# Kernel tuning notes

Measured on AMD Instinct MI355X. Metric: run time of the kernel, lower is better.

## Reference

```python
import jax, jax.numpy as jnp
import numpy as np

# Module/problem constants (match init_kwargs & input_specs)
B, D, H, W = 2, 96, 96, 96
CIN, COUT, K = 16, 32, 3
N = 200000  # number of active (sparse) voxels


def setup_inputs() -> dict:
    key = jax.random.key(0)
    kf, kw, kb = jax.random.split(key, 3)
    # unique valid voxel coordinates -> deterministic scatter semantics
    rng = np.random.default_rng(0)
    lin = rng.choice(B * D * H * W, size=N, replace=False)
    b, z, y, x = np.unravel_index(lin, (B, D, H, W))
    indices = jnp.asarray(np.stack([b, z, y, x], axis=1).astype(np.int32))  # [N,4]
    features = jax.random.normal(kf, (N, CIN), dtype=jnp.float32)
    fan_in = CIN * K ** 3
    conv_w = jax.random.normal(kw, (COUT, CIN, K, K, K), dtype=jnp.float32) / np.sqrt(fan_in)
    conv_b = jax.random.normal(kb, (COUT,), dtype=jnp.float32) * 0.01
    return {"features": features, "indices": indices, "conv_w": conv_w, "conv_b": conv_b}


def reference(features, indices, conv_w, conv_b):
    """DenseFallbackConv3d.forward on a SparseConvTensor, stride=1 path.

    1) scatter sparse features into dense grid [B,CIN,D,H,W]
    2) dense Conv3d (k=3, pad=1, stride=1) + bias
    3) gather per-point output features at the same voxel indices -> [N,COUT]
    """
    b = indices[:, 0]
    z = indices[:, 1]
    y = indices[:, 2]
    x = indices[:, 3]
    # scatter: equivalent of grid[b, :, z, y, x] = features
    grid = jnp.zeros((B, CIN, D, H, W), dtype=features.dtype).at[b, :, z, y, x].set(features)
    out = jax.lax.conv_general_dilated(
        grid, conv_w,
        window_strides=(1, 1, 1),
        padding=((1, 1), (1, 1), (1, 1)),
        dimension_numbers=("NCDHW", "OIDHW", "NCDHW"),
    )
    out = out + conv_b[None, :, None, None, None]
    # gather: out_dense[b, :, z, y, x] for every active voxel -> [N, COUT]
    return out[b, :, z, y, x]
```

## Files before the change

### kernel.cpp

```cpp
#include <hip/hip_runtime.h>

#define BB   2
#define DD   96
#define HH   96
#define WW   96
#define CINC 16
#define COUTC 32
#define KVOL 27
#define GRID_VOX (BB*DD*HH*WW)
#define NW (KVOL*CINC*COUTC)
#define VPT 8
#define CVB (256*VPT)

typedef _Float16 half8 __attribute__((ext_vector_type(8)));
typedef float    floatx16 __attribute__((ext_vector_type(16)));

__global__ __launch_bounds__(256) void setup_kernel(
        const int* __restrict__ idx, int* __restrict__ g,
        const float* __restrict__ w, _Float16* __restrict__ wH,
        int* __restrict__ counter, int n, int scatter_blocks) {
    if ((int)blockIdx.x < scatter_blocks) {
        int i = blockIdx.x * 256 + threadIdx.x;
        if (i >= n) return;
        int4 v = ((const int4*)idx)[i];
        int lin = ((v.x * DD + v.y) * HH + v.z) * WW + v.w;
        g[lin] = i;
    } else {
        int t = ((int)blockIdx.x - scatter_blocks) * 256 + threadIdx.x;
        if (t == 0) counter[0] = 0;
        if (t >= NW) return;
        int ci = t & (CINC - 1);
        int co = (t >> 4) & (COUTC - 1);
        int kk = t >> 9;
        wH[t] = (_Float16)w[(co * CINC + ci) * KVOL + kk];
    }
}

__global__ __launch_bounds__(256) void compact_kernel(
        const int* __restrict__ idx, const float* __restrict__ feat,
        int* __restrict__ g, _Float16* __restrict__ featH,
        int* __restrict__ pc, int* __restrict__ perm,
        int* __restrict__ counter, int n) {
    __shared__ int s_off[256];
    __shared__ int s_base;
    const int t = threadIdx.x;
    const int base = blockIdx.x * CVB + t * VPT;

    int4 a0 = ((const int4*)(g + base))[0];
    int4 a1 = ((const int4*)(g + base))[1];
    int vals[VPT] = {a0.x, a0.y, a0.z, a0.w, a1.x, a1.y, a1.z, a1.w};
    int pid[VPT], pck[VPT];
    int cnt = 0;
#pragma unroll
    for (int q = 0; q < VPT; ++q) {
        int p = vals[q];
        bool ok = ((unsigned)p < (unsigned)n);
        int pk = 0;
        if (ok) {
            int4 c = ((const int4*)idx)[p];
            int lin = ((c.x * DD + c.y) * HH + c.z) * WW + c.w;
            ok = (lin == base + q);
            pk = (c.x << 21) | (c.y << 14) | (c.z << 7) | c.w;
        }
        pid[q] = ok ? p : -1;
        pck[q] = pk;
        cnt += ok ? 1 : 0;
    }

    s_off[t] = cnt;
    __syncthreads();
    for (int d = 1; d < 256; d <<= 1) {
        int v = (t >= d) ? s_off[t - d] : 0;
        __syncthreads();
        s_off[t] += v;
        __syncthreads();
    }
    if (t == 255) s_base = atomicAdd(counter, s_off[255]);
    __syncthreads();
    int o = s_base + s_off[t] - cnt;

#pragma unroll
    for (int q = 0; q < VPT; ++q) {
        int tag = n;
        int p = pid[q];
        if (p >= 0) {
            pc[o] = pck[q];
            perm[o] = p;
            const float4* src = (const float4*)(feat + (size_t)p * CINC);
            float4 f0 = src[0], f1 = src[1], f2 = src[2], f3 = src[3];
            half8 h0, h1;
            h0[0]=(_Float16)f0.x; h0[1]=(_Float16)f0.y; h0[2]=(_Float16)f0.z; h0[3]=(_Float16)f0.w;
            h0[4]=(_Float16)f1.x; h0[5]=(_Float16)f1.y; h0[6]=(_Float16)f1.z; h0[7]=(_Float16)f1.w;
            h1[0]=(_Float16)f2.x; h1[1]=(_Float16)f2.y; h1[2]=(_Float16)f2.z; h1[3]=(_Float16)f2.w;
            h1[4]=(_Float16)f3.x; h1[5]=(_Float16)f3.y; h1[6]=(_Float16)f3.z; h1[7]=(_Float16)f3.w;
            half8* dst = (half8*)(featH + (size_t)o * CINC);
            dst[0] = h0; dst[1] = h1;
            tag = o;
            ++o;
        }
        g[base + q] = tag;
    }
    if (blockIdx.x == 0 && t == 0) {
        half8* zr = (half8*)(featH + (size_t)n * CINC);
        half8 hz = {};
        zr[0] = hz; zr[1] = hz;
    }
}

__global__ __launch_bounds__(256) void conv_mfma_kernel(
        const _Float16* __restrict__ featH, const int* __restrict__ pc,
        const int* __restrict__ perm, const _Float16* __restrict__ wH,
        const float* __restrict__ bias, const int* __restrict__ g,
        float* __restrict__ out, int n) {
    const int lane = threadIdx.x & 63;
    const int wave = threadIdx.x >> 6;
    const int m    = lane & 31;
    const int hf   = lane >> 5;
    const int j0   = (blockIdx.x * 4 + wave) * 32;
    if (j0 >= n) return;
    const int j = j0 + m;

    const int p = pc[j];
    const int x = p & 127, y = (p >> 7) & 127, z = (p >> 14) & 127, b = p >> 21;
    const int base = ((b * DD + z) * HH + y) * WW + x;
    const int pm = perm[j];

    int nid[KVOL];
#pragma unroll
    for (int kk = 0; kk < KVOL; ++kk) {
        const int dz = kk / 9 - 1, dy = (kk / 3) % 3 - 1, dx = kk % 3 - 1;
        int nz = z + dz, ny = y + dy, nx = x + dx;
        bool inb = ((unsigned)nz < DD) & ((unsigned)ny < HH) & ((unsigned)nx < WW);
        int addr = inb ? base + (dz * HH + dy) * WW + dx : 0;
        int v = g[addr];
        nid[kk] = inb ? v : n;
    }

    float bval = bias[m];
    floatx16 acc;
#pragma unroll
    for (int i = 0; i < 16; ++i) acc[i] = bval;

#pragma unroll
    for (int kk = 0; kk < KVOL; ++kk) {
        half8 a = *(const half8*)(featH + (size_t)nid[kk] * CINC + hf * 8);
        half8 bf = *(const half8*)(wH + kk * (COUTC * CINC) + m * CINC + hf * 8);
        acc = __builtin_amdgcn_mfma_f32_32x32x16_f16(a, bf, acc, 0, 0, 0);
    }

#pragma unroll
    for (int i = 0; i < 16; ++i) {
        int r = (i & 3) + 8 * (i >> 2) + 4 * hf;
        int row = __shfl(pm, r);
        out[(size_t)row * COUTC + m] = acc[i];
    }
}

extern "C" void kernel_launch(void* const* d_in, const int* in_sizes, int n_in,
                              void* d_out, int out_size, void* d_ws, size_t ws_size,
                              hipStream_t stream) {
    const float* feat  = (const float*)d_in[0];
    const int*   idx   = (const int*)d_in[1];
    const float* convw = (const float*)d_in[2];
    const float* convb = (const float*)d_in[3];
    float* out = (float*)d_out;

    const int n = in_sizes[1] / 4;

    char* ws = (char*)d_ws;
    int*      g       = (int*)ws;
    int*      counter = (int*)(ws + GRID_VOX * 4);
    int*      pc      = (int*)(ws + GRID_VOX * 4 + 256);
    int*      perm    = pc + n;
    _Float16* featH   = (_Float16*)(perm + n);
    _Float16* wH      = featH + (size_t)(n + 1) * CINC;

    hipMemsetAsync(g, 0xFF, (size_t)GRID_VOX * sizeof(int), stream);

    const int sb = (n + 255) / 256;
    const int rb = (NW + 255) / 256;
    setup_kernel<<<sb + rb, 256, 0, stream>>>(idx, g, convw, wH, counter, n, sb);
    compact_kernel<<<GRID_VOX / CVB, 256, 0, stream>>>(
        idx, feat, g, featH, pc, perm, counter, n);

    const int waves = (n + 31) / 32;
    conv_mfma_kernel<<<(waves + 3) / 4, 256, 0, stream>>>(
        featH, pc, perm, wH, convb, g, out, n);
}
```

Measured before the change: 127.9 us.

## Stage weights in LDS, batch neighbor loads, use wave scan, and drop grid memset

The conv kernel now copies the fp16 weights into padded shared memory once per block and reads the B operand from LDS. It also issues the nine neighbor feature loads of each group before their MFMAs, so more loads are in flight at once. The compaction kernel replaces its LDS Hillis-Steele scan, which had many barriers, with a wave-level shuffle scan plus a 4-entry combine. The memset of the dense index grid is removed, relying on the existing idx-based validation to reject stale or garbage entries. The trade-off is an LDS-fill prologue per block and higher register pressure from holding nine feature vectors.

```diff
diff --git a/kernel.cpp b/kernel.cpp
--- a/kernel.cpp
+++ b/kernel.cpp
@@ -11,6 +11,7 @@
 #define NW (KVOL*CINC*COUTC)
 #define VPT 8
 #define CVB (256*VPT)
+#define SWP 24
 
 typedef _Float16 half8 __attribute__((ext_vector_type(8)));
 typedef float    floatx16 __attribute__((ext_vector_type(16)));
@@ -41,9 +42,12 @@
         int* __restrict__ g, _Float16* __restrict__ featH,
         int* __restrict__ pc, int* __restrict__ perm,
         int* __restrict__ counter, int n) {
-    __shared__ int s_off[256];
+    __shared__ int s_wsum[4];
+    __shared__ int s_wbase[4];
     __shared__ int s_base;
     const int t = threadIdx.x;
+    const int lane = t & 63;
+    const int wv = t >> 6;
     const int base = blockIdx.x * CVB + t * VPT;
 
     int4 a0 = ((const int4*)(g + base))[0];
@@ -67,17 +71,22 @@
         cnt += ok ? 1 : 0;
     }
 
-    s_off[t] = cnt;
+    int incl = cnt;
+#pragma unroll
+    for (int d = 1; d < 64; d <<= 1) {
+        int v = __shfl_up(incl, d);
+        if (lane >= d) incl += v;
+    }
+    if (lane == 63) s_wsum[wv] = incl;
     __syncthreads();
-    for (int d = 1; d < 256; d <<= 1) {
-        int v = (t >= d) ? s_off[t - d] : 0;
-        __syncthreads();
-        s_off[t] += v;
-        __syncthreads();
-    }
-    if (t == 255) s_base = atomicAdd(counter, s_off[255]);
+    if (t == 0) {
+        int t0 = s_wsum[0], t1 = s_wsum[1], t2 = s_wsum[2], t3 = s_wsum[3];
+        s_wbase[0] = 0; s_wbase[1] = t0; s_wbase[2] = t0 + t1;
+        s_wbase[3] = t0 + t1 + t2;
+        s_base = atomicAdd(counter, t0 + t1 + t2 + t3);
+    }
     __syncthreads();
-    int o = s_base + s_off[t] - cnt;
+    int o = s_base + s_wbase[wv] + incl - cnt;
 
 #pragma unroll
     for (int q = 0; q < VPT; ++q) {
@@ -112,11 +121,21 @@
         const int* __restrict__ perm, const _Float16* __restrict__ wH,
         const float* __restrict__ bias, const int* __restrict__ g,
         float* __restrict__ out, int n) {
+    __shared__ _Float16 sW[KVOL * 32 * SWP];
     const int lane = threadIdx.x & 63;
     const int wave = threadIdx.x >> 6;
     const int m    = lane & 31;
     const int hf   = lane >> 5;
-    const int j0   = (blockIdx.x * 4 + wave) * 32;
+
+    for (int u = threadIdx.x; u < KVOL * 64; u += 256) {
+        int kk = u >> 6, r = u & 63;
+        int co = r >> 1, h = r & 1;
+        half8 v = *(const half8*)(wH + kk * (COUTC * CINC) + co * CINC + h * 8);
+        *(half8*)(&sW[kk * 32 * SWP + co * SWP + h * 8]) = v;
+    }
+    __syncthreads();
+
+    const int j0 = (blockIdx.x * 4 + wave) * 32;
     if (j0 >= n) return;
     const int j = j0 + m;
 
@@ -142,10 +161,17 @@
     for (int i = 0; i < 16; ++i) acc[i] = bval;
 
 #pragma unroll
-    for (int kk = 0; kk < KVOL; ++kk) {
-        half8 a = *(const half8*)(featH + (size_t)nid[kk] * CINC + hf * 8);
-        half8 bf = *(const half8*)(wH + kk * (COUTC * CINC) + m * CINC + hf * 8);
-        acc = __builtin_amdgcn_mfma_f32_32x32x16_f16(a, bf, acc, 0, 0, 0);
+    for (int gq = 0; gq < 3; ++gq) {
+        half8 av[9];
+#pragma unroll
+        for (int q = 0; q < 9; ++q)
+            av[q] = *(const half8*)(featH + (size_t)nid[gq * 9 + q] * CINC + hf * 8);
+#pragma unroll
+        for (int q = 0; q < 9; ++q) {
+            const int kk = gq * 9 + q;
+            half8 bf = *(const half8*)(&sW[kk * 32 * SWP + m * SWP + hf * 8]);
+            acc = __builtin_amdgcn_mfma_f32_32x32x16_f16(av[q], bf, acc, 0, 0, 0);
+        }
     }
 
 #pragma unroll
@@ -175,8 +201,6 @@
     _Float16* featH   = (_Float16*)(perm + n);
     _Float16* wH      = featH + (size_t)(n + 1) * CINC;
 
-    hipMemsetAsync(g, 0xFF, (size_t)GRID_VOX * sizeof(int), stream);
-
     const int sb = (n + 255) / 256;
     const int rb = (NW + 255) / 256;
     setup_kernel<<<sb + rb, 256, 0, stream>>>(idx, g, convw, wH, counter, n, sb);
```

After: 122.4 us. -4.3%, faster.
